# Kernel tuning notes

Hardware: AMD Instinct MI355X
Metric: run time of the kernel (lower is better)

Reference implementation:

```python
import jax, jax.numpy as jnp
import numpy as np

NUM_HEADS = 4
STEPS_PER_DAY = 288
NUM_LAYERS = 3


def _ln(x, g, b):
    mu = jnp.mean(x, -1, keepdims=True)
    var = jnp.mean((x - mu) ** 2, -1, keepdims=True)
    return (x - mu) * jax.lax.rsqrt(var + 1e-5) * g + b


def _mha(x, Wq, bq, Wk, bk, Wv, bv, Wo, bo):
    # x: (B, S, L, D); attention over L (the -2 dim), matching AttentionLayer
    B, S, L, D = x.shape
    hd = D // NUM_HEADS
    q = (x @ Wq + bq).reshape(B, S, L, NUM_HEADS, hd)
    k = (x @ Wk + bk).reshape(B, S, L, NUM_HEADS, hd)
    v = (x @ Wv + bv).reshape(B, S, L, NUM_HEADS, hd)
    s = jnp.einsum('bslhd,bsmhd->bshlm', q, k) * (hd ** -0.5)
    a = jax.nn.softmax(s, axis=-1)
    o = jnp.einsum('bshlm,bsmhd->bslhd', a, v).reshape(B, S, L, D)
    return o @ Wo + bo


def _sal(x, params, i, dim):
    # SelfAttentionLayer (eval mode: dropout = identity)
    Wq, bq, Wk, bk, Wv, bv, Wo, bo, W1, b1, W2, b2, g1, B1, g2, B2 = (p[i] for p in params)
    x = jnp.swapaxes(x, dim, -2)
    x = _ln(x + _mha(x, Wq, bq, Wk, bk, Wv, bv, Wo, bo), g1, B1)
    x = _ln(x + (jax.nn.relu(x @ W1 + b1) @ W2 + b2), g2, B2)
    return jnp.swapaxes(x, dim, -2)


def _forward(x, W_in, b_in, tod_emb, dow_emb, node_emb, adp_emb, tparams, sparams, Wout, bout):
    B, T, N, _ = x.shape
    tod_idx = jnp.clip((x[..., 1] * STEPS_PER_DAY).astype(jnp.int32), 0, STEPS_PER_DAY - 1)
    dow_idx = jnp.clip(x[..., 2].astype(jnp.int32), 0, 6)
    h = jnp.concatenate([
        x @ W_in + b_in,                                    # input_proj (B,T,N,24)
        tod_emb[tod_idx],                                   # (B,T,N,24)
        dow_emb[dow_idx],                                   # (B,T,N,24)
        jnp.broadcast_to(node_emb, (B, T, N, node_emb.shape[-1])),
        jnp.broadcast_to(adp_emb, (B,) + adp_emb.shape),    # (B,T,N,80)
    ], axis=-1)                                             # model_dim = 176
    for i in range(NUM_LAYERS):
        h = _sal(h, tparams, i, 1)   # temporal attention over in_steps
    for i in range(NUM_LAYERS):
        h = _sal(h, sparams, i, 2)   # spatial attention over nodes
    out = jnp.swapaxes(h, 1, 2).reshape(B, N, -1) @ Wout + bout  # (B,N,out_steps)
    return jnp.swapaxes(out.reshape(B, N, -1, 1), 1, 2)          # (B,out_steps,N,1)


def setup_inputs() -> dict:
    ks = iter(jax.random.split(jax.random.key(0), 80))
    B, T, N, D, L, FF = 32, 12, 307, 176, NUM_LAYERS, 256
    nrm = lambda *s: jax.random.normal(next(ks), s, jnp.float32) * 0.02
    x0 = jax.random.normal(next(ks), (B, T, N, 1), jnp.float32)   # traffic value
    tod = jax.random.uniform(next(ks), (B, T, N, 1), jnp.float32)  # tod fraction in [0,1)
    dow = jax.random.uniform(next(ks), (B, T, N, 1), jnp.float32) * 6.99  # dow in [0,7)
    inp = {'x': jnp.concatenate([x0, tod, dow], -1),
           'W_in': nrm(3, 24), 'b_in': nrm(24),
           'tod_emb': nrm(STEPS_PER_DAY, 24), 'dow_emb': nrm(7, 24),
           'node_emb': nrm(N, 24), 'adp_emb': nrm(T, N, 80),
           'Wout': nrm(T * D, 12), 'bout': nrm(12)}
    shapes = {'Wq': (L, D, D), 'bq': (L, D), 'Wk': (L, D, D), 'bk': (L, D),
              'Wv': (L, D, D), 'bv': (L, D), 'Wo': (L, D, D), 'bo': (L, D),
              'W1': (L, D, FF), 'b1': (L, FF), 'W2': (L, FF, D), 'b2': (L, D)}
    for pfx in ('t', 's'):
        for nm, sh in shapes.items():
            inp[pfx + nm] = nrm(*sh)
        inp[pfx + 'g1'] = jnp.ones((L, D)); inp[pfx + 'B1'] = jnp.zeros((L, D))
        inp[pfx + 'g2'] = jnp.ones((L, D)); inp[pfx + 'B2'] = jnp.zeros((L, D))
    return inp


def reference(x, W_in, b_in, tod_emb, dow_emb, node_emb, adp_emb,
              tWq, tbq, tWk, tbk, tWv, tbv, tWo, tbo, tW1, tb1, tW2, tb2, tg1, tB1, tg2, tB2,
              sWq, sbq, sWk, sbk, sWv, sbv, sWo, sbo, sW1, sb1, sW2, sb2, sg1, sB1, sg2, sB2,
              Wout, bout):
    tparams = (tWq, tbq, tWk, tbk, tWv, tbv, tWo, tbo, tW1, tb1, tW2, tb2, tg1, tB1, tg2, tB2)
    sparams = (sWq, sbq, sWk, sbk, sWv, sbv, sWo, sbo, sW1, sb1, sW2, sb2, sg1, sB1, sg2, sB2)
    return _forward(x, W_in, b_in, tod_emb, dow_emb, node_emb, adp_emb, tparams, sparams, Wout, bout)
```

## Files before the change

kernel.cpp:

```cpp
#include <hip/hip_runtime.h>

#define BB 32
#define TPB 3684L
#define TT 12
#define NN 307
#define DM 176
#define KP 192
#define FFD 256
#define NH 4
#define HD 44
#define NTILE 77
#define TS 584

typedef __bf16 bfv8 __attribute__((ext_vector_type(8)));
typedef float f32x4 __attribute__((ext_vector_type(4)));
typedef short sv4 __attribute__((ext_vector_type(4)));
typedef unsigned int uiv4 __attribute__((ext_vector_type(4)));
typedef unsigned long long ull;

__device__ __forceinline__ float b2f(unsigned short h) {
  return __uint_as_float(((unsigned)h) << 16);
}
__device__ __forceinline__ unsigned short f2b(float f) {
  unsigned u = __float_as_uint(f);
  return (unsigned short)((u + 0x7FFFu + ((u >> 16) & 1u)) >> 16);
}

__device__ __forceinline__ f32x4 mfma16x16x16bf(sv4 a, sv4 b, f32x4 c) {
#if __has_builtin(__builtin_amdgcn_mfma_f32_16x16x16bf16_1k)
  return __builtin_amdgcn_mfma_f32_16x16x16bf16_1k(a, b, c, 0, 0, 0);
#else
  f32x4 d = c;
  asm("v_mfma_f32_16x16x16_bf16 %0, %1, %2, %0\n\ts_nop 7\n\ts_nop 7"
      : "+v"(d) : "v"(a), "v"(b));
  return d;
#endif
}

__global__ void prep_weights(
    const float* __restrict__ tWq, const float* __restrict__ tWk,
    const float* __restrict__ tWv, const float* __restrict__ tWo,
    const float* __restrict__ tW1, const float* __restrict__ tW2,
    const float* __restrict__ sWq, const float* __restrict__ sWk,
    const float* __restrict__ sWv, const float* __restrict__ sWo,
    const float* __restrict__ sW1, const float* __restrict__ sW2,
    const float* __restrict__ tbq, const float* __restrict__ tbk,
    const float* __restrict__ tbv,
    const float* __restrict__ sbq, const float* __restrict__ sbk,
    const float* __restrict__ sbv,
    unsigned short* __restrict__ wbase, float* __restrict__ bqkv) {
  int layer = blockIdx.y;
  int mat = blockIdx.z;
  int li = layer % 3;
  bool tp = (layer < 3);
  unsigned short* dst = wbase + (long)layer * 229376;
  long idx = (long)blockIdx.x * 256 + threadIdx.x;
  if (mat == 0) {
    if (idx < 528 * 192) {
      int nn = idx / 192, k = idx % 192;
      float v = 0.f;
      if (k < 176) {
        int sel = nn / 176, c = nn % 176;
        const float* W = tp ? (sel == 0 ? tWq : sel == 1 ? tWk : tWv)
                            : (sel == 0 ? sWq : sel == 1 ? sWk : sWv);
        v = W[(long)li * 176 * 176 + k * 176 + c];
      }
      dst[idx] = f2b(v);
    }
    if (idx < 528) {
      int sel = idx / 176, c = idx % 176;
      const float* bb = tp ? (sel == 0 ? tbq : sel == 1 ? tbk : tbv)
                           : (sel == 0 ? sbq : sel == 1 ? sbk : sbv);
      bqkv[layer * 528 + idx] = bb[li * 176 + c];
    }
  } else if (mat == 1) {
    if (idx < 176 * 192) {
      int nn = idx / 192, k = idx % 192;
      int hh = k / 48, dd = k % 48;
      float v = (dd < 44)
          ? (tp ? tWo : sWo)[(long)li * 176 * 176 + (hh * 44 + dd) * 176 + nn]
          : 0.f;
      dst[101376 + idx] = f2b(v);
    }
  } else if (mat == 2) {
    if (idx < 256 * 192) {
      int nn = idx / 192, k = idx % 192;
      float v = (k < 176) ? (tp ? tW1 : sW1)[(long)li * 176 * 256 + k * 256 + nn] : 0.f;
      dst[135168 + idx] = f2b(v);
    }
  } else {
    if (idx < 176 * 256) {
      int nn = idx / 256, k = idx % 256;
      float v = (tp ? tW2 : sW2)[(long)li * 256 * 176 + k * 176 + nn];
      dst[184320 + idx] = f2b(v);
    }
  }
}

__global__ __launch_bounds__(256) void embed_kernel(
    const float* __restrict__ x, const float* __restrict__ W_in,
    const float* __restrict__ b_in, const float* __restrict__ tod,
    const float* __restrict__ dow, const float* __restrict__ node,
    const float* __restrict__ adp, float* __restrict__ h,
    unsigned short* __restrict__ hb, long tok0, long Mc) {
  long i = (long)blockIdx.x * 256 + threadIdx.x;
  if (i >= Mc * KP) return;
  int dp = (int)(i % KP);
  long tok = i / KP;
  if (dp >= DM) { hb[tok * KP + dp] = 0; return; }
  long tg = tok0 + tok;
  int n = (int)(tg % NN);
  long bt = tg / NN;
  int t = (int)(bt % TT);
  float v;
  int d = dp;
  if (d < 24) {
    const float* xp = x + tg * 3;
    v = xp[0] * W_in[d] + xp[1] * W_in[24 + d] + xp[2] * W_in[48 + d] + b_in[d];
  } else if (d < 48) {
    float x1 = x[tg * 3 + 1];
    int idx = (int)(x1 * 288.0f);
    idx = idx < 0 ? 0 : (idx > 287 ? 287 : idx);
    v = tod[idx * 24 + (d - 24)];
  } else if (d < 72) {
    float x2 = x[tg * 3 + 2];
    int idx = (int)x2;
    idx = idx < 0 ? 0 : (idx > 6 ? 6 : idx);
    v = dow[idx * 24 + (d - 48)];
  } else if (d < 96) {
    v = node[n * 24 + (d - 72)];
  } else {
    v = adp[((long)t * NN + n) * 80 + (d - 96)];
  }
  h[tok * DM + d] = v;
  hb[tok * KP + d] = f2b(v);
}

template <int KSTEPS, bool RELU, bool OUTBF16, bool QKVPAD, bool AHM>
__global__ __launch_bounds__(256) void gemm_bias(
    const unsigned short* __restrict__ A, int lda,
    const unsigned short* __restrict__ Wt, const float* __restrict__ bias,
    void* __restrict__ out, int ldo, long M, int N, int tpy, long PS) {
  int wave = threadIdx.x >> 6;
  int lane = threadIdx.x & 63;
  long wrow = ((long)blockIdx.x * 4 + wave) * 64;
  if (wrow >= M) return;
  int lrow = lane & 15;
  int kq = lane >> 4;
  bfv8 a[4][KSTEPS];
#pragma unroll
  for (int rf = 0; rf < 4; ++rf) {
    long ar = wrow + rf * 16 + lrow;
    if (ar >= M) ar = M - 1;
#pragma unroll
    for (int ks = 0; ks < KSTEPS; ++ks) {
      if (AHM) {
        int kp0 = ks * 32 + kq * 8;
        int hh = kp0 / 48;
        int off = kp0 - hh * 48;
        a[rf][ks] = *(const bfv8*)(A + (long)hh * PS + ar * 48 + off);
      } else {
        a[rf][ks] = *(const bfv8*)(A + ar * (long)lda + kq * 8 + ks * 32);
      }
    }
  }
  int ntiles = N >> 4;
  int nt0 = blockIdx.y * tpy;
  int ntE = nt0 + tpy;
  if (ntE > ntiles) ntE = ntiles;
  for (int nt = nt0; nt < ntE; ++nt) {
    int col = nt * 16 + lrow;
    const unsigned short* bp = Wt + (long)col * lda + kq * 8;
    f32x4 acc[4] = {{0, 0, 0, 0}, {0, 0, 0, 0}, {0, 0, 0, 0}, {0, 0, 0, 0}};
#pragma unroll
    for (int ks = 0; ks < KSTEPS; ++ks) {
      bfv8 b = *(const bfv8*)(bp + ks * 32);
#pragma unroll
      for (int rf = 0; rf < 4; ++rf)
        acc[rf] = __builtin_amdgcn_mfma_f32_16x16x32_bf16(a[rf][ks], b, acc[rf], 0, 0, 0);
    }
    float bv = bias[col];
    long obase = 0;
    int ocol = col;
    if (QKVPAD) {
      int sel = col / 176, rem = col - sel * 176;
      int hh = rem / 44, dd = rem - hh * 44;
      obase = (long)(sel * 4 + hh) * PS;
      ocol = dd;
    }
#pragma unroll
    for (int rf = 0; rf < 4; ++rf) {
      long r0 = wrow + rf * 16 + kq * 4;
#pragma unroll
      for (int r = 0; r < 4; ++r) {
        if (r0 + r >= M) continue;
        float v = acc[rf][r] + bv;
        if (RELU) v = fmaxf(v, 0.f);
        long idx = QKVPAD ? (obase + (r0 + r) * 48 + ocol)
                          : ((r0 + r) * (long)ldo + ocol);
        if (OUTBF16)
          ((unsigned short*)out)[idx] = f2b(v);
        else
          ((float*)out)[idx] = v;
      }
    }
  }
  if (QKVPAD && blockIdx.y == 0) {
    long row = wrow + lane;
    if (row < M) {
#pragma unroll
      for (int p = 0; p < 12; ++p)
        *(ull*)((unsigned short*)out + (long)p * PS + row * 48 + 44) = 0ULL;
    }
  }
}

__global__ __launch_bounds__(256) void attn_temporal_lds(
    const unsigned short* __restrict__ qkvh, unsigned short* __restrict__ atth,
    long PS) {
  __shared__ unsigned short ld[4 * 12 * TS];
  int tile = blockIdx.x % NTILE;
  int b = blockIdx.x / NTILE;
  int n0 = tile * 4;
  for (int idx = threadIdx.x; idx < 3456; idx += 256) {
    int p = idx / 288;
    int rem = idx % 288;
    int t = rem / 24;
    int rem2 = rem % 24;
    int j = rem2 / 6, e = rem2 % 6;
    uiv4 v = {0, 0, 0, 0};
    int n = n0 + j;
    if (n < NN)
      v = *(const uiv4*)(qkvh + (long)p * PS + ((long)(b * TT + t) * NN + n) * 48 + e * 8);
    *(uiv4*)(&ld[(j * 12 + p) * TS + t * 48 + e * 8]) = v;
  }
  __syncthreads();
  int tid = threadIdx.x;
  if (tid >= 192) return;
  int j = tid / 48, hl = tid % 48;
  int hh = hl / 12, l = hl % 12;
  int n = n0 + j;
  if (n >= NN) return;
  const float scale = 0.15075567228888181f;
  float q[HD];
  const unsigned short* qp = &ld[(j * 12 + hh) * TS + l * 48];
#pragma unroll
  for (int d = 0; d < HD; ++d) q[d] = b2f(qp[d]) * scale;
  float s[TT];
  float mx = -1e30f;
#pragma unroll
  for (int m = 0; m < TT; ++m) {
    const unsigned short* kp = &ld[(j * 12 + 4 + hh) * TS + m * 48];
    float acc = 0.f;
#pragma unroll
    for (int d = 0; d < HD; ++d) acc += q[d] * b2f(kp[d]);
    s[m] = acc;
    mx = fmaxf(mx, acc);
  }
  float den = 0.f;
#pragma unroll
  for (int m = 0; m < TT; ++m) { s[m] = __expf(s[m] - mx); den += s[m]; }
  float inv = 1.f / den;
  float o[HD];
#pragma unroll
  for (int d = 0; d < HD; ++d) o[d] = 0.f;
#pragma unroll
  for (int m = 0; m < TT; ++m) {
    const unsigned short* vp = &ld[(j * 12 + 8 + hh) * TS + m * 48];
    float p = s[m] * inv;
#pragma unroll
    for (int d = 0; d < HD; ++d) o[d] += p * b2f(vp[d]);
  }
  unsigned short* op = atth + (long)hh * PS + ((long)(b * TT + l) * NN + n) * 48;
#pragma unroll
  for (int d = 0; d < HD; d += 2) {
    unsigned u = (unsigned)f2b(o[d]) | ((unsigned)f2b(o[d + 1]) << 16);
    *(unsigned*)(op + d) = u;
  }
  *(ull*)(op + 44) = 0ULL;
}

#define KLS 72
#define VTS 332
__global__ __launch_bounds__(512, 2) void attn_spatial_mfma(
    const unsigned short* __restrict__ qkvh, unsigned short* __restrict__ atth,
    long PS) {
  __shared__ unsigned short Kl[320 * KLS];
  __shared__ unsigned short Vt[48 * VTS];
  int h = blockIdx.x & 3;
  int bt = blockIdx.x >> 2;
  long tokbase = (long)bt * NN;
  const unsigned short* qbase = qkvh + (long)h * PS + tokbase * 48;
  const unsigned short* kbase = qkvh + (long)(4 + h) * PS + tokbase * 48;
  const unsigned short* vbase = qkvh + (long)(8 + h) * PS + tokbase * 48;
  int tid = threadIdx.x;

  for (int idx = tid; idx < 320 * 8; idx += 512) {
    int m = idx >> 3, c = idx & 7;
    uiv4 v = {0, 0, 0, 0};
    if (c < 6 && m < NN) v = *(const uiv4*)(kbase + (long)m * 48 + c * 8);
    *(uiv4*)(&Kl[m * KLS + c * 8]) = v;
  }
  for (int task = tid; task < 480; task += 512) {
    int m0 = (task / 6) * 4, c = task % 6;
    const unsigned short* vb = vbase + c * 8;
    uiv4 r0 = {0, 0, 0, 0}, r1 = {0, 0, 0, 0}, r2 = {0, 0, 0, 0}, r3 = {0, 0, 0, 0};
    if (m0 + 0 < NN) r0 = *(const uiv4*)(vb + (long)(m0 + 0) * 48);
    if (m0 + 1 < NN) r1 = *(const uiv4*)(vb + (long)(m0 + 1) * 48);
    if (m0 + 2 < NN) r2 = *(const uiv4*)(vb + (long)(m0 + 2) * 48);
    if (m0 + 3 < NN) r3 = *(const uiv4*)(vb + (long)(m0 + 3) * 48);
#pragma unroll
    for (int j = 0; j < 8; ++j) {
      int w32 = j >> 1, sh = (j & 1) * 16;
      ull o = (ull)((r0[w32] >> sh) & 0xFFFFu) |
              ((ull)((r1[w32] >> sh) & 0xFFFFu) << 16) |
              ((ull)((r2[w32] >> sh) & 0xFFFFu) << 32) |
              ((ull)((r3[w32] >> sh) & 0xFFFFu) << 48);
      *(ull*)(&Vt[(c * 8 + j) * VTS + m0]) = o;
    }
  }
  __syncthreads();

  int w = tid >> 6;
  int lane = tid & 63;
  int lrow = lane & 15;
  int kq = lane >> 4;
  const float kscale = 0.2174944602f;

#pragma unroll
  for (int qi = 0; qi < 3; ++qi) {
    int qt = qi * 8 + w;
    if (qt >= 20) break;
    int ql = qt * 16 + lrow;
    int qc = ql < NN ? ql : NN - 1;
    const unsigned short* qrow = qbase + (long)qc * 48;
    bfv8 qb8a = *(const bfv8*)(qrow + kq * 8);
    bfv8 qb8b = *(const bfv8*)(qrow + 32 + kq * 8);

    float m_run = -1e30f, den = 0.f;
    f32x4 o0 = {0.f, 0.f, 0.f, 0.f}, o1 = {0.f, 0.f, 0.f, 0.f}, o2 = {0.f, 0.f, 0.f, 0.f};
#pragma unroll
    for (int ct = 0; ct < 20; ++ct) {
      const unsigned short* kp = &Kl[(ct * 16 + lrow) * KLS];
      bfv8 k8a = *(const bfv8*)(kp + kq * 8);
      bfv8 k8b = *(const bfv8*)(kp + 32 + kq * 8);
      f32x4 s = {0.f, 0.f, 0.f, 0.f};
      s = __builtin_amdgcn_mfma_f32_16x16x32_bf16(k8a, qb8a, s, 0, 0, 0);
      s = __builtin_amdgcn_mfma_f32_16x16x32_bf16(k8b, qb8b, s, 0, 0, 0);
#pragma unroll
      for (int r = 0; r < 4; ++r) {
        float v = s[r] * kscale;
        if (ct == 19 && (kq * 4 + r) >= 3) v = -1e30f;
        s[r] = v;
      }
      float smax = fmaxf(fmaxf(s[0], s[1]), fmaxf(s[2], s[3]));
      if (!__all(smax <= m_run + 8.f)) {
        smax = fmaxf(smax, __shfl_xor(smax, 16));
        smax = fmaxf(smax, __shfl_xor(smax, 32));
        float m_new = fmaxf(m_run, smax);
        float corr = exp2f(m_run - m_new);
        m_run = m_new;
        den *= corr;
        o0 = o0 * corr;
        o1 = o1 * corr;
        o2 = o2 * corr;
      }
      float p0 = exp2f(s[0] - m_run);
      float p1 = exp2f(s[1] - m_run);
      float p2 = exp2f(s[2] - m_run);
      float p3 = exp2f(s[3] - m_run);
      den += (p0 + p1) + (p2 + p3);
      sv4 pb = {(short)f2b(p0), (short)f2b(p1), (short)f2b(p2), (short)f2b(p3)};
      int mb = ct * 16 + kq * 4;
      sv4 a0 = *(const sv4*)(&Vt[(0 * 16 + lrow) * VTS + mb]);
      sv4 a1 = *(const sv4*)(&Vt[(1 * 16 + lrow) * VTS + mb]);
      sv4 a2 = *(const sv4*)(&Vt[(2 * 16 + lrow) * VTS + mb]);
      o0 = mfma16x16x16bf(a0, pb, o0);
      o1 = mfma16x16x16bf(a1, pb, o1);
      o2 = mfma16x16x16bf(a2, pb, o2);
    }
    den += __shfl_xor(den, 16);
    den += __shfl_xor(den, 32);
    float inv = 1.f / den;

    if (ql < NN) {
      unsigned short* dst = atth + (long)h * PS + (tokbase + ql) * 48;
      int db = kq * 4;
      {
        ull u = (ull)f2b(o0[0] * inv) | ((ull)f2b(o0[1] * inv) << 16) |
                ((ull)f2b(o0[2] * inv) << 32) | ((ull)f2b(o0[3] * inv) << 48);
        *(ull*)(dst + db) = u;
      }
      {
        ull u = (ull)f2b(o1[0] * inv) | ((ull)f2b(o1[1] * inv) << 16) |
                ((ull)f2b(o1[2] * inv) << 32) | ((ull)f2b(o1[3] * inv) << 48);
        *(ull*)(dst + 16 + db) = u;
      }
      if (db < 12) {
        ull u = (ull)f2b(o2[0] * inv) | ((ull)f2b(o2[1] * inv) << 16) |
                ((ull)f2b(o2[2] * inv) << 32) | ((ull)f2b(o2[3] * inv) << 48);
        *(ull*)(dst + 32 + db) = u;
      } else {
        *(ull*)(dst + 44) = 0ULL;
      }
    }
  }
}

__global__ __launch_bounds__(256) void ln_kernel(
    const float* hin, const float* __restrict__ res,
    const float* __restrict__ g, const float* __restrict__ beta,
    float* hout, unsigned short* __restrict__ hb, long M) {
  long tok = (long)blockIdx.x * 4 + (threadIdx.x >> 6);
  if (tok >= M) return;
  int lane = threadIdx.x & 63;
  float r[3];
  float sum = 0.f, ss = 0.f;
#pragma unroll
  for (int j = 0; j < 3; ++j) {
    int d = j * 64 + lane;
    float v = 0.f;
    if (d < DM) v = hin[tok * DM + d] + res[tok * DM + d];
    r[j] = v;
    sum += v;
    ss += v * v;
  }
#pragma unroll
  for (int o = 32; o > 0; o >>= 1) {
    sum += __shfl_xor(sum, o);
    ss += __shfl_xor(ss, o);
  }
  float mean = sum * (1.f / 176.f);
  float var = ss * (1.f / 176.f) - mean * mean;
  float rstd = rsqrtf(var + 1e-5f);
#pragma unroll
  for (int j = 0; j < 3; ++j) {
    int d = j * 64 + lane;
    if (d < DM) {
      float y = (r[j] - mean) * rstd * g[d] + beta[d];
      hout[tok * DM + d] = y;
      hb[tok * KP + d] = f2b(y);
    } else if (d < KP) {
      hb[tok * KP + d] = 0;
    }
  }
}

__global__ __launch_bounds__(64) void out_kernel(
    const float* __restrict__ h, const float* __restrict__ Wout,
    const float* __restrict__ bout, float* __restrict__ out, int b0) {
  int bn = blockIdx.x;
  int n = bn % NN, bl = bn / NN;
  int b = b0 + bl;
  int lane = threadIdx.x;
  float acc[TT];
#pragma unroll
  for (int j = 0; j < TT; ++j) acc[j] = 0.f;
  for (int k = lane; k < TT * DM; k += 64) {
    int t = k / DM, d = k % DM;
    float a = h[((long)(bl * TT + t) * NN + n) * DM + d];
    const float* wp = Wout + (long)k * TT;
#pragma unroll
    for (int j = 0; j < TT; ++j) acc[j] += a * wp[j];
  }
#pragma unroll
  for (int j = 0; j < TT; ++j)
    for (int o = 32; o > 0; o >>= 1) acc[j] += __shfl_xor(acc[j], o);
  if (lane < TT) out[((long)b * TT + lane) * NN + n] = acc[lane] + bout[lane];
}

extern "C" void kernel_launch(void* const* d_in, const int* in_sizes, int n_in,
                              void* d_out, int out_size, void* d_ws, size_t ws_size,
                              hipStream_t stream) {
  char* ws = (char*)d_ws;
  unsigned short* wbase = (unsigned short*)ws;
  float* bqkv = (float*)(ws + 2752512L);
  char* dyn = ws + 2765184L;

  const long per_tok = 2752;
  int nb = 0;
  for (int c = 32; c >= 1; --c) {
    if (2765184L + (long)c * TPB * per_tok <= (long)ws_size) { nb = c; break; }
  }
  if (nb == 0) return;

  const long Mal = (long)nb * TPB;
  const long PS = Mal * 48;
  float* h = (float*)dyn;
  unsigned short* hb = (unsigned short*)(dyn + Mal * 704);
  unsigned short* atth = hb;
  unsigned short* qkvh = (unsigned short*)(dyn + Mal * 1088);
  float* proj = (float*)(dyn + Mal * 1088);
  unsigned short* mid = (unsigned short*)(dyn + Mal * 2240);

#define DF(i) ((const float*)d_in[i])

  prep_weights<<<dim3(396, 6, 4), 256, 0, stream>>>(
      DF(9), DF(11), DF(13), DF(15), DF(17), DF(19),
      DF(25), DF(27), DF(29), DF(31), DF(33), DF(35),
      DF(10), DF(12), DF(14), DF(26), DF(28), DF(30), wbase, bqkv);

  for (int b0 = 0; b0 < BB; b0 += nb) {
    int nb_cur = (BB - b0 < nb) ? (BB - b0) : nb;
    const long Mc = (long)nb_cur * TPB;
    int gx = (int)((Mc + 255) / 256);
    int ln_blocks = (int)((Mc + 3) / 4);

    embed_kernel<<<(int)((Mc * KP + 255) / 256), 256, 0, stream>>>(
        DF(0), DF(1), DF(2), DF(3), DF(4), DF(5), DF(6), h, hb,
        (long)b0 * TPB, Mc);

    for (int l = 0; l < 6; ++l) {
      int base = (l < 3) ? 9 : 25;
      int li = l % 3;
      const unsigned short* wl = wbase + (long)l * 229376;
      const unsigned short* Wqkv = wl;
      const unsigned short* Wo = wl + 101376;
      const unsigned short* W1 = wl + 135168;
      const unsigned short* W2 = wl + 184320;
      const float* bo = DF(base + 7) + li * 176;
      const float* b1 = DF(base + 9) + li * 256;
      const float* b2 = DF(base + 11) + li * 176;
      const float* g1 = DF(base + 12) + li * 176;
      const float* B1 = DF(base + 13) + li * 176;
      const float* g2 = DF(base + 14) + li * 176;
      const float* B2 = DF(base + 15) + li * 176;

      gemm_bias<6, false, true, true, false><<<dim3(gx, 3), 256, 0, stream>>>(
          hb, KP, Wqkv, bqkv + l * 528, qkvh, 0, Mc, 528, 11, PS);

      if (l < 3) {
        attn_temporal_lds<<<nb_cur * NTILE, 256, 0, stream>>>(qkvh, atth, PS);
      } else {
        attn_spatial_mfma<<<nb_cur * TT * NH, 512, 0, stream>>>(qkvh, atth, PS);
      }

      gemm_bias<6, false, false, false, true><<<dim3(gx, 2), 256, 0, stream>>>(
          atth, KP, Wo, bo, proj, DM, Mc, DM, 6, PS);

      ln_kernel<<<ln_blocks, 256, 0, stream>>>(h, proj, g1, B1, h, hb, Mc);

      gemm_bias<6, true, true, false, false><<<dim3(gx, 2), 256, 0, stream>>>(
          hb, KP, W1, b1, mid, FFD, Mc, FFD, 8, 0);

      gemm_bias<8, false, false, false, false><<<dim3(gx, 2), 256, 0, stream>>>(
          mid, FFD, W2, b2, proj, DM, Mc, DM, 6, 0);

      ln_kernel<<<ln_blocks, 256, 0, stream>>>(h, proj, g2, B2, h, hb, Mc);
    }

    out_kernel<<<nb_cur * NN, 64, 0, stream>>>(h, DF(7), DF(8), (float*)d_out, b0);
  }
#undef DF
}
```

Baseline: 3.711 ms.

## Fuse output-projection and FFN2 GEMMs with residual add and LayerNorm

Replaces the Wo GEMM + LN kernel and W2 GEMM + LN kernel pairs with a single fused kernel per pair. Each block computes 64 rows across all 176 output columns over 4 waves, adds bias and residual, reduces row statistics through shared memory, and writes normalized fp32 and bf16 activations. This removes the fp32 proj intermediate round trip and two launches per layer, and shrinks the workspace per token so more batches fit per chunk. In exchange the fused GEMM has a 64-row block with per-wave column tiles, which changes occupancy and parallelism, and buffer aliasing is reorganized (mid shares space with qkvh, atth moves).

```diff
diff --git a/kernel.cpp b/kernel.cpp
--- a/kernel.cpp
+++ b/kernel.cpp
@@ -136,7 +136,7 @@
   hb[tok * KP + d] = f2b(v);
 }
 
-template <int KSTEPS, bool RELU, bool OUTBF16, bool QKVPAD, bool AHM>
+template <int KSTEPS, bool RELU, bool OUTBF16, bool QKVPAD>
 __global__ __launch_bounds__(256) void gemm_bias(
     const unsigned short* __restrict__ A, int lda,
     const unsigned short* __restrict__ Wt, const float* __restrict__ bias,
@@ -153,16 +153,8 @@
     long ar = wrow + rf * 16 + lrow;
     if (ar >= M) ar = M - 1;
 #pragma unroll
-    for (int ks = 0; ks < KSTEPS; ++ks) {
-      if (AHM) {
-        int kp0 = ks * 32 + kq * 8;
-        int hh = kp0 / 48;
-        int off = kp0 - hh * 48;
-        a[rf][ks] = *(const bfv8*)(A + (long)hh * PS + ar * 48 + off);
-      } else {
-        a[rf][ks] = *(const bfv8*)(A + ar * (long)lda + kq * 8 + ks * 32);
-      }
-    }
+    for (int ks = 0; ks < KSTEPS; ++ks)
+      a[rf][ks] = *(const bfv8*)(A + ar * (long)lda + kq * 8 + ks * 32);
   }
   int ntiles = N >> 4;
   int nt0 = blockIdx.y * tpy;
@@ -211,6 +203,132 @@
 #pragma unroll
       for (int p = 0; p < 12; ++p)
         *(ull*)((unsigned short*)out + (long)p * PS + row * 48 + 44) = 0ULL;
+    }
+  }
+}
+
+template <int KSTEPS, bool AHM>
+__global__ __launch_bounds__(256) void gemm_ln_fused(
+    const unsigned short* __restrict__ A, int lda,
+    const unsigned short* __restrict__ Wt, const float* __restrict__ bias,
+    const float* __restrict__ g, const float* __restrict__ beta,
+    float* __restrict__ h, unsigned short* __restrict__ hb,
+    long M, long PS) {
+  __shared__ float2 part[64][5];
+  int w = threadIdx.x >> 6;
+  int lane = threadIdx.x & 63;
+  long wrow = (long)blockIdx.x * 64;
+  if (wrow >= M) return;
+  int lrow = lane & 15;
+  int kq = lane >> 4;
+  bfv8 a[4][KSTEPS];
+#pragma unroll
+  for (int rf = 0; rf < 4; ++rf) {
+    long ar = wrow + rf * 16 + lrow;
+    if (ar >= M) ar = M - 1;
+#pragma unroll
+    for (int ks = 0; ks < KSTEPS; ++ks) {
+      if (AHM) {
+        int kp0 = ks * 32 + kq * 8;
+        int hh = kp0 / 48;
+        int off = kp0 - hh * 48;
+        a[rf][ks] = *(const bfv8*)(A + (long)hh * PS + ar * 48 + off);
+      } else {
+        a[rf][ks] = *(const bfv8*)(A + ar * (long)lda + kq * 8 + ks * 32);
+      }
+    }
+  }
+  f32x4 acc[3][4];
+#pragma unroll
+  for (int i = 0; i < 3; ++i) {
+    int nt = w + 4 * i;
+    if (nt >= 11) continue;
+    int col = nt * 16 + lrow;
+    const unsigned short* bp = Wt + (long)col * lda + kq * 8;
+    f32x4 c0 = {0, 0, 0, 0}, c1 = {0, 0, 0, 0}, c2 = {0, 0, 0, 0}, c3 = {0, 0, 0, 0};
+#pragma unroll
+    for (int ks = 0; ks < KSTEPS; ++ks) {
+      bfv8 b = *(const bfv8*)(bp + ks * 32);
+      c0 = __builtin_amdgcn_mfma_f32_16x16x32_bf16(a[0][ks], b, c0, 0, 0, 0);
+      c1 = __builtin_amdgcn_mfma_f32_16x16x32_bf16(a[1][ks], b, c1, 0, 0, 0);
+      c2 = __builtin_amdgcn_mfma_f32_16x16x32_bf16(a[2][ks], b, c2, 0, 0, 0);
+      c3 = __builtin_amdgcn_mfma_f32_16x16x32_bf16(a[3][ks], b, c3, 0, 0, 0);
+    }
+    acc[i][0] = c0; acc[i][1] = c1; acc[i][2] = c2; acc[i][3] = c3;
+  }
+  float sum[16], ss[16];
+#pragma unroll
+  for (int j = 0; j < 16; ++j) { sum[j] = 0.f; ss[j] = 0.f; }
+#pragma unroll
+  for (int i = 0; i < 3; ++i) {
+    int nt = w + 4 * i;
+    if (nt >= 11) continue;
+    int col = nt * 16 + lrow;
+    float bv = bias[col];
+#pragma unroll
+    for (int rf = 0; rf < 4; ++rf)
+#pragma unroll
+      for (int r = 0; r < 4; ++r) {
+        long row = wrow + rf * 16 + kq * 4 + r;
+        long rr = row < M ? row : M - 1;
+        float v = acc[i][rf][r] + bv + h[rr * DM + col];
+        acc[i][rf][r] = v;
+        sum[rf * 4 + r] += v;
+        ss[rf * 4 + r] += v * v;
+      }
+  }
+#pragma unroll
+  for (int j = 0; j < 16; ++j) {
+#pragma unroll
+    for (int o = 1; o < 16; o <<= 1) {
+      sum[j] += __shfl_xor(sum[j], o);
+      ss[j] += __shfl_xor(ss[j], o);
+    }
+  }
+  if (lrow == 0) {
+#pragma unroll
+    for (int rf = 0; rf < 4; ++rf)
+#pragma unroll
+      for (int r = 0; r < 4; ++r)
+        part[rf * 16 + kq * 4 + r][w] = float2{sum[rf * 4 + r], ss[rf * 4 + r]};
+  }
+  __syncthreads();
+  if (w == 0) {
+    float s = 0.f, q = 0.f;
+#pragma unroll
+    for (int ww = 0; ww < 4; ++ww) {
+      float2 p = part[lane][ww];
+      s += p.x; q += p.y;
+    }
+    float mean = s * (1.f / 176.f);
+    float var = q * (1.f / 176.f) - mean * mean;
+    part[lane][4] = float2{mean, rsqrtf(var + 1e-5f)};
+  }
+  __syncthreads();
+#pragma unroll
+  for (int i = 0; i < 3; ++i) {
+    int nt = w + 4 * i;
+    if (nt >= 11) continue;
+    int col = nt * 16 + lrow;
+    float gv = g[col], bv2 = beta[col];
+#pragma unroll
+    for (int rf = 0; rf < 4; ++rf)
+#pragma unroll
+      for (int r = 0; r < 4; ++r) {
+        int lr = rf * 16 + kq * 4 + r;
+        long row = wrow + lr;
+        if (row >= M) continue;
+        float2 st = part[lr][4];
+        float y = (acc[i][rf][r] - st.x) * st.y * gv + bv2;
+        h[row * DM + col] = y;
+        hb[row * KP + col] = f2b(y);
+      }
+  }
+  if (w == 0) {
+    long row = wrow + lane;
+    if (row < M) {
+      ull* zp = (ull*)(hb + row * KP + DM);
+      zp[0] = 0ULL; zp[1] = 0ULL; zp[2] = 0ULL; zp[3] = 0ULL;
     }
   }
 }
@@ -407,45 +525,6 @@
   }
 }
 
-__global__ __launch_bounds__(256) void ln_kernel(
-    const float* hin, const float* __restrict__ res,
-    const float* __restrict__ g, const float* __restrict__ beta,
-    float* hout, unsigned short* __restrict__ hb, long M) {
-  long tok = (long)blockIdx.x * 4 + (threadIdx.x >> 6);
-  if (tok >= M) return;
-  int lane = threadIdx.x & 63;
-  float r[3];
-  float sum = 0.f, ss = 0.f;
-#pragma unroll
-  for (int j = 0; j < 3; ++j) {
-    int d = j * 64 + lane;
-    float v = 0.f;
-    if (d < DM) v = hin[tok * DM + d] + res[tok * DM + d];
-    r[j] = v;
-    sum += v;
-    ss += v * v;
-  }
-#pragma unroll
-  for (int o = 32; o > 0; o >>= 1) {
-    sum += __shfl_xor(sum, o);
-    ss += __shfl_xor(ss, o);
-  }
-  float mean = sum * (1.f / 176.f);
-  float var = ss * (1.f / 176.f) - mean * mean;
-  float rstd = rsqrtf(var + 1e-5f);
-#pragma unroll
-  for (int j = 0; j < 3; ++j) {
-    int d = j * 64 + lane;
-    if (d < DM) {
-      float y = (r[j] - mean) * rstd * g[d] + beta[d];
-      hout[tok * DM + d] = y;
-      hb[tok * KP + d] = f2b(y);
-    } else if (d < KP) {
-      hb[tok * KP + d] = 0;
-    }
-  }
-}
-
 __global__ __launch_bounds__(64) void out_kernel(
     const float* __restrict__ h, const float* __restrict__ Wout,
     const float* __restrict__ bout, float* __restrict__ out, int b0) {
@@ -477,7 +556,7 @@
   float* bqkv = (float*)(ws + 2752512L);
   char* dyn = ws + 2765184L;
 
-  const long per_tok = 2752;
+  const long per_tok = 2624;
   int nb = 0;
   for (int c = 32; c >= 1; --c) {
     if (2765184L + (long)c * TPB * per_tok <= (long)ws_size) { nb = c; break; }
@@ -488,10 +567,9 @@
   const long PS = Mal * 48;
   float* h = (float*)dyn;
   unsigned short* hb = (unsigned short*)(dyn + Mal * 704);
-  unsigned short* atth = hb;
   unsigned short* qkvh = (unsigned short*)(dyn + Mal * 1088);
-  float* proj = (float*)(dyn + Mal * 1088);
-  unsigned short* mid = (unsigned short*)(dyn + Mal * 2240);
+  unsigned short* mid = qkvh;
+  unsigned short* atth = (unsigned short*)(dyn + Mal * 2240);
 
 #define DF(i) ((const float*)d_in[i])
 
@@ -504,7 +582,7 @@
     int nb_cur = (BB - b0 < nb) ? (BB - b0) : nb;
     const long Mc = (long)nb_cur * TPB;
     int gx = (int)((Mc + 255) / 256);
-    int ln_blocks = (int)((Mc + 3) / 4);
+    int gx64 = (int)((Mc + 63) / 64);
 
     embed_kernel<<<(int)((Mc * KP + 255) / 256), 256, 0, stream>>>(
         DF(0), DF(1), DF(2), DF(3), DF(4), DF(5), DF(6), h, hb,
@@ -526,7 +604,7 @@
       const float* g2 = DF(base + 14) + li * 176;
       const float* B2 = DF(base + 15) + li * 176;
 
-      gemm_bias<6, false, true, true, false><<<dim3(gx, 3), 256, 0, stream>>>(
+      gemm_bias<6, false, true, true><<<dim3(gx, 3), 256, 0, stream>>>(
           hb, KP, Wqkv, bqkv + l * 528, qkvh, 0, Mc, 528, 11, PS);
 
       if (l < 3) {
@@ -535,18 +613,14 @@
         attn_spatial_mfma<<<nb_cur * TT * NH, 512, 0, stream>>>(qkvh, atth, PS);
       }
 
-      gemm_bias<6, false, false, false, true><<<dim3(gx, 2), 256, 0, stream>>>(
-          atth, KP, Wo, bo, proj, DM, Mc, DM, 6, PS);
-
-      ln_kernel<<<ln_blocks, 256, 0, stream>>>(h, proj, g1, B1, h, hb, Mc);
-
-      gemm_bias<6, true, true, false, false><<<dim3(gx, 2), 256, 0, stream>>>(
+      gemm_ln_fused<6, true><<<gx64, 256, 0, stream>>>(
+          atth, KP, Wo, bo, g1, B1, h, hb, Mc, PS);
+
+      gemm_bias<6, true, true, false><<<dim3(gx, 2), 256, 0, stream>>>(
           hb, KP, W1, b1, mid, FFD, Mc, FFD, 8, 0);
 
-      gemm_bias<8, false, false, false, false><<<dim3(gx, 2), 256, 0, stream>>>(
-          mid, FFD, W2, b2, proj, DM, Mc, DM, 6, 0);
-
-      ln_kernel<<<ln_blocks, 256, 0, stream>>>(h, proj, g2, B2, h, hb, Mc);
+      gemm_ln_fused<8, false><<<gx64, 256, 0, stream>>>(
+          mid, FFD, W2, b2, g2, B2, h, hb, Mc, 0);
     }
 
     out_kernel<<<nb_cur * NN, 64, 0, stream>>>(h, DF(7), DF(8), (float*)d_out, b0);
```

Measured after the change: 3.673 ms. Within noise of the previous version (-1.0%).
